# Performance work log

Measured on AMD Instinct MI355X. Metric: run time of the kernel, lower is better.

## Reference

```python
import jax, jax.numpy as jnp
import numpy as np

WINDOW_LEN = 512
N_VAR = 64
LOW_RANK = 16
BATCH = 512


def setup_inputs() -> dict:
    key = jax.random.key(0)
    k_x, k_g, k_b, k_A, k_B = jax.random.split(key, 5)
    x = jax.random.normal(k_x, (BATCH, WINDOW_LEN, N_VAR, 1), dtype=jnp.float32)
    # gating initialized at gating_init in the module; use small positive values
    gating = 0.01 * jnp.ones((N_VAR,), dtype=jnp.float32)
    # bias initialized to zeros in the module, but give it random values so the
    # residual path is exercised numerically
    bias = 0.02 * jax.random.normal(k_b, (WINDOW_LEN, N_VAR), dtype=jnp.float32)
    # kaiming-uniform-ish scale for lora_A: bound = sqrt(6 / fan_in) / sqrt(1+a^2) with a=sqrt(5)
    bound = np.sqrt(6.0 / LOW_RANK) / np.sqrt(6.0)
    lora_A = jax.random.uniform(k_A, (WINDOW_LEN, LOW_RANK), dtype=jnp.float32,
                                minval=-bound, maxval=bound)
    # lora_B is zero-init in the module; use small random values for a nontrivial test
    lora_B = 0.02 * jax.random.normal(k_B, (LOW_RANK, WINDOW_LEN, N_VAR), dtype=jnp.float32)
    return {"x": x, "gating": gating, "bias": bias, "lora_A": lora_A, "lora_B": lora_B}


def reference(x, gating, bias, lora_A, lora_B):
    # x: [b, t, n, d] with t == window_len and n*d == n_var (var_wise=True path)
    b, t, n, d = x.shape
    xr = x.reshape(b, t, n * d)                     # [b, t, v]
    x1 = jnp.tanh(gating * xr)                      # gate per variable, [b, t, v]
    # Original computes weight = einsum('ik,kjl->ijl', lora_A, lora_B)  (dense [t,t,v])
    # then einsum('biv,iov->bov', x1, weight). Same math via associativity:
    tmp = jnp.einsum('biv,ik->bkv', x1, lora_A)     # [b, r, v]
    new_x = jnp.einsum('bkv,kov->bov', tmp, lora_B) # [b, t, v]
    out = xr + new_x + bias                          # residual + bias
    return out.reshape(b, t, n, d)
```

## Files before the change

kernel.cpp:

```cpp
#include <hip/hip_runtime.h>

#define WL 512
#define NV 64
#define LR 16
#define NB 512
#define BB 8
#define OO 8

__device__ __forceinline__ float tanh_fast(float x) {
    float e = __expf(2.0f * x);
    return 1.0f - 2.0f / (e + 1.0f);
}

__global__ __launch_bounds__(1024, 8) void k_tmp(
    const float* __restrict__ x, const float* __restrict__ gating,
    const float* __restrict__ A, float* __restrict__ tmp)
{
    __shared__ float red[16 * LR * NV];
    const int tid = threadIdx.x;
    const int b = blockIdx.x;

    const int v = tid & 63;
    const int tg = __builtin_amdgcn_readfirstlane(tid >> 6);
    const float g = gating[v];

    float acc[LR];
#pragma unroll
    for (int k = 0; k < LR; ++k) acc[k] = 0.f;

    const float* xb = x + (size_t)b * (WL * NV) + (size_t)tg * 32 * NV + v;
    const float* Abase = A + (size_t)tg * 32 * LR;

#pragma unroll 4
    for (int i = 0; i < 32; ++i) {
        const float x1 = tanh_fast(g * xb[i * NV]);
        const float* Ar = Abase + i * LR;
#pragma unroll
        for (int k = 0; k < LR; ++k) acc[k] = fmaf(x1, Ar[k], acc[k]);
    }

#pragma unroll
    for (int k = 0; k < LR; ++k) red[(tg * LR + k) * NV + v] = acc[k];
    __syncthreads();

    {
        const int p = tid;
        float s = 0.f;
#pragma unroll
        for (int t = 0; t < 16; ++t) s += red[t * (LR * NV) + p];
        tmp[(size_t)b * (LR * NV) + p] = s;
    }
}

__global__ __attribute__((amdgpu_flat_work_group_size(256, 256),
                          amdgpu_waves_per_eu(2, 2)))
void k_out(
    const float* __restrict__ x, const float* __restrict__ bias,
    const float* __restrict__ Bm, const float* __restrict__ tmp,
    float* __restrict__ out)
{
    __shared__ float B_lds[OO * LR * NV];
    __shared__ float T_lds[BB * LR * NV];
    const int tid = threadIdx.x;
    const int v = tid & 63;
    const int wv = tid >> 6;
    const int o0 = blockIdx.y * OO;
    const int b0 = blockIdx.x * BB;

#pragma unroll
    for (int i = 0; i < 8; ++i) {
        const int fidx = i * 256 + tid;
        const int ko = fidx >> 4;
        const int v4 = fidx & 15;
        const int ol = ko >> 4;
        const int k  = ko & 15;
        const float4 val = *(const float4*)(Bm + ((size_t)k * WL + (o0 + ol)) * NV + v4 * 4);
        *(float4*)(B_lds + ((ol * LR + k) * NV) + v4 * 4) = val;
    }
    {
        const float4* src = (const float4*)(tmp + (size_t)b0 * (LR * NV));
        float4* dst = (float4*)T_lds;
#pragma unroll
        for (int i = 0; i < 8; ++i) dst[i * 256 + tid] = src[i * 256 + tid];
    }
    __syncthreads();

    const int ol0 = wv * 2;
    float Breg[2][LR];
#pragma unroll
    for (int j = 0; j < 2; ++j)
#pragma unroll
        for (int k = 0; k < LR; ++k)
            Breg[j][k] = B_lds[((ol0 + j) * LR + k) * NV + v];
    float breg[2];
#pragma unroll
    for (int j = 0; j < 2; ++j) breg[j] = bias[(o0 + ol0 + j) * NV + v];

    float xr[2], xrn[2];
    {
        const float* xb = x + (size_t)b0 * (WL * NV);
#pragma unroll
        for (int j = 0; j < 2; ++j) xr[j] = xb[(o0 + ol0 + j) * NV + v];
    }

    for (int bl = 0; bl < BB; ++bl) {
        const int b = b0 + bl;
        if (bl + 1 < BB) {
            const float* xb = x + (size_t)(b + 1) * (WL * NV);
#pragma unroll
            for (int j = 0; j < 2; ++j) xrn[j] = xb[(o0 + ol0 + j) * NV + v];
        }

        float tr[LR];
#pragma unroll
        for (int k = 0; k < LR; ++k) tr[k] = T_lds[(bl * LR + k) * NV + v];

        float* ob = out + (size_t)b * (WL * NV);
#pragma unroll
        for (int j = 0; j < 2; ++j) {
            float acc = breg[j];
#pragma unroll
            for (int k = 0; k < LR; ++k) acc += tr[k] * Breg[j][k];
            ob[(o0 + ol0 + j) * NV + v] = xr[j] + acc;
        }

        if (bl + 1 < BB) { xr[0] = xrn[0]; xr[1] = xrn[1]; }
    }
}

extern "C" void kernel_launch(void* const* d_in, const int* in_sizes, int n_in,
                              void* d_out, int out_size, void* d_ws, size_t ws_size,
                              hipStream_t stream) {
    const float* x      = (const float*)d_in[0];
    const float* gating = (const float*)d_in[1];
    const float* bias   = (const float*)d_in[2];
    const float* A      = (const float*)d_in[3];
    const float* Bm     = (const float*)d_in[4];
    float* out = (float*)d_out;
    float* tmp = (float*)d_ws;

    k_tmp<<<NB, 1024, 0, stream>>>(x, gating, A, tmp);
    k_out<<<dim3(64, 64), 256, 0, stream>>>(x, bias, Bm, tmp, out);
}
```

Before: 51.56 us.

## Transpose tmp layout, stream it from global per batch, and double batches per block

k_tmp now writes tmp in [b][v][k] order and pads its reduction buffer to 65 columns so the transposed reads avoid LDS bank conflicts. k_out drops the T_lds staging and has each thread load its 16 tmp values directly as four float4 loads, prefetching the next batch alongside x. BB goes from 8 to 16, halving the grid and the number of B tile reloads, and the waves-per-EU hint rises to 4 now that LDS use is lower. In exchange each block does longer serial work, and the per-thread float4 loads of tmp are strided by 64 bytes across lanes rather than fully coalesced.

```diff
diff --git a/kernel.cpp b/kernel.cpp
--- a/kernel.cpp
+++ b/kernel.cpp
@@ -4,7 +4,7 @@
 #define NV 64
 #define LR 16
 #define NB 512
-#define BB 8
+#define BB 16
 #define OO 8
 
 __device__ __forceinline__ float tanh_fast(float x) {
@@ -16,7 +16,7 @@
     const float* __restrict__ x, const float* __restrict__ gating,
     const float* __restrict__ A, float* __restrict__ tmp)
 {
-    __shared__ float red[16 * LR * NV];
+    __shared__ float red[16 * LR * 65];
     const int tid = threadIdx.x;
     const int b = blockIdx.x;
 
@@ -40,27 +40,28 @@
     }
 
 #pragma unroll
-    for (int k = 0; k < LR; ++k) red[(tg * LR + k) * NV + v] = acc[k];
+    for (int k = 0; k < LR; ++k) red[(tg * LR + k) * 65 + v] = acc[k];
     __syncthreads();
 
     {
         const int p = tid;
+        const int v2 = p >> 4;
+        const int k2 = p & 15;
         float s = 0.f;
 #pragma unroll
-        for (int t = 0; t < 16; ++t) s += red[t * (LR * NV) + p];
-        tmp[(size_t)b * (LR * NV) + p] = s;
+        for (int t = 0; t < 16; ++t) s += red[(t * LR + k2) * 65 + v2];
+        tmp[(size_t)b * (LR * NV) + v2 * LR + k2] = s;
     }
 }
 
 __global__ __attribute__((amdgpu_flat_work_group_size(256, 256),
-                          amdgpu_waves_per_eu(2, 2)))
+                          amdgpu_waves_per_eu(4, 4)))
 void k_out(
     const float* __restrict__ x, const float* __restrict__ bias,
     const float* __restrict__ Bm, const float* __restrict__ tmp,
     float* __restrict__ out)
 {
     __shared__ float B_lds[OO * LR * NV];
-    __shared__ float T_lds[BB * LR * NV];
     const int tid = threadIdx.x;
     const int v = tid & 63;
     const int wv = tid >> 6;
@@ -77,12 +78,6 @@
         const float4 val = *(const float4*)(Bm + ((size_t)k * WL + (o0 + ol)) * NV + v4 * 4);
         *(float4*)(B_lds + ((ol * LR + k) * NV) + v4 * 4) = val;
     }
-    {
-        const float4* src = (const float4*)(tmp + (size_t)b0 * (LR * NV));
-        float4* dst = (float4*)T_lds;
-#pragma unroll
-        for (int i = 0; i < 8; ++i) dst[i * 256 + tid] = src[i * 256 + tid];
-    }
     __syncthreads();
 
     const int ol0 = wv * 2;
@@ -96,24 +91,35 @@
 #pragma unroll
     for (int j = 0; j < 2; ++j) breg[j] = bias[(o0 + ol0 + j) * NV + v];
 
-    float xr[2], xrn[2];
+    float4 t4a[4], t4b[4];
+    float xra[2], xrb[2];
     {
+        const float4* tb = (const float4*)(tmp + (size_t)b0 * (LR * NV) + v * LR);
+#pragma unroll
+        for (int q = 0; q < 4; ++q) t4a[q] = tb[q];
         const float* xb = x + (size_t)b0 * (WL * NV);
 #pragma unroll
-        for (int j = 0; j < 2; ++j) xr[j] = xb[(o0 + ol0 + j) * NV + v];
+        for (int j = 0; j < 2; ++j) xra[j] = xb[(o0 + ol0 + j) * NV + v];
     }
 
+#pragma unroll 1
     for (int bl = 0; bl < BB; ++bl) {
         const int b = b0 + bl;
+
         if (bl + 1 < BB) {
+            const float4* tb = (const float4*)(tmp + (size_t)(b + 1) * (LR * NV) + v * LR);
+#pragma unroll
+            for (int q = 0; q < 4; ++q) t4b[q] = tb[q];
             const float* xb = x + (size_t)(b + 1) * (WL * NV);
 #pragma unroll
-            for (int j = 0; j < 2; ++j) xrn[j] = xb[(o0 + ol0 + j) * NV + v];
+            for (int j = 0; j < 2; ++j) xrb[j] = xb[(o0 + ol0 + j) * NV + v];
         }
 
         float tr[LR];
-#pragma unroll
-        for (int k = 0; k < LR; ++k) tr[k] = T_lds[(bl * LR + k) * NV + v];
+        tr[0]=t4a[0].x; tr[1]=t4a[0].y; tr[2]=t4a[0].z; tr[3]=t4a[0].w;
+        tr[4]=t4a[1].x; tr[5]=t4a[1].y; tr[6]=t4a[1].z; tr[7]=t4a[1].w;
+        tr[8]=t4a[2].x; tr[9]=t4a[2].y; tr[10]=t4a[2].z; tr[11]=t4a[2].w;
+        tr[12]=t4a[3].x; tr[13]=t4a[3].y; tr[14]=t4a[3].z; tr[15]=t4a[3].w;
 
         float* ob = out + (size_t)b * (WL * NV);
 #pragma unroll
@@ -121,10 +127,14 @@
             float acc = breg[j];
 #pragma unroll
             for (int k = 0; k < LR; ++k) acc += tr[k] * Breg[j][k];
-            ob[(o0 + ol0 + j) * NV + v] = xr[j] + acc;
+            ob[(o0 + ol0 + j) * NV + v] = xra[j] + acc;
         }
 
-        if (bl + 1 < BB) { xr[0] = xrn[0]; xr[1] = xrn[1]; }
+        if (bl + 1 < BB) {
+#pragma unroll
+            for (int q = 0; q < 4; ++q) t4a[q] = t4b[q];
+            xra[0] = xrb[0]; xra[1] = xrb[1];
+        }
     }
 }
 
@@ -140,5 +150,5 @@
     float* tmp = (float*)d_ws;
 
     k_tmp<<<NB, 1024, 0, stream>>>(x, gating, A, tmp);
-    k_out<<<dim3(64, 64), 256, 0, stream>>>(x, bias, Bm, tmp, out);
+    k_out<<<dim3(32, 64), 256, 0, stream>>>(x, bias, Bm, tmp, out);
 }
```

After: 59.20 us. 1.15x slower.
